# Performance work log

Measured on AMD Instinct MI355X. Metric: run time of the kernel, lower is better.

## Reference

```python
import jax, jax.numpy as jnp
import numpy as np
import math

B, S, D, H = 4, 2048, 1024, 16
DK = D // H  # 64
THETA = 10000.0


def setup_inputs() -> dict:
    key = jax.random.key(0)
    ks = jax.random.split(key, 5)
    std = 0.02
    return {
        "x": jax.random.normal(ks[0], (B, S, D), dtype=jnp.float32),
        "Wq": jax.random.normal(ks[1], (D, D), dtype=jnp.float32) * std,
        "Wk": jax.random.normal(ks[2], (D, D), dtype=jnp.float32) * std,
        "Wv": jax.random.normal(ks[3], (D, D), dtype=jnp.float32) * std,
        "Wo": jax.random.normal(ks[4], (D, D), dtype=jnp.float32) * std / math.sqrt(2 * 12),
        "token_positions": jnp.arange(S, dtype=jnp.int32),
    }


def _rope(x, pos):
    # x: [B, H, S, DK]; pos: [S]. Interleaved-pair rotary embedding.
    inv_freq = THETA ** (-jnp.arange(0, DK, 2, dtype=jnp.float32) / DK)  # [DK/2]
    ang = pos.astype(jnp.float32)[:, None] * inv_freq[None, :]  # [S, DK/2]
    cos, sin = jnp.cos(ang), jnp.sin(ang)
    x1, x2 = x[..., 0::2], x[..., 1::2]  # [B, H, S, DK/2]
    r1 = x1 * cos - x2 * sin
    r2 = x1 * sin + x2 * cos
    return jnp.stack([r1, r2], axis=-1).reshape(x.shape)


def reference(x, Wq, Wk, Wv, Wo, token_positions):
    b, s, d = x.shape
    Q = x @ Wq
    K = x @ Wk
    V = x @ Wv
    # [B, S, D] -> [B, H, S, DK]
    def split(t):
        return t.reshape(b, s, H, DK).transpose(0, 2, 1, 3)
    Qh, Kh, Vh = split(Q), split(K), split(V)
    Qh = _rope(Qh, token_positions)
    Kh = _rope(Kh, token_positions)
    scores = jnp.einsum('bhqd,bhkd->bhqk', Qh, Kh) / math.sqrt(DK)
    causal = jnp.tril(jnp.ones((s, s), dtype=bool))
    scores = jnp.where(causal, scores, -jnp.inf)
    probs = jax.nn.softmax(scores, axis=-1)
    out = jnp.einsum('bhqk,bhkd->bhqd', probs, Vh)
    out = out.transpose(0, 2, 1, 3).reshape(b, s, d)
    return out @ Wo
```

## Files before the change

kernel.cpp:

```cpp
#include <hip/hip_runtime.h>
#include <hip/hip_bf16.h>

#define B_N 4
#define S_LEN 2048
#define D_MODEL 1024
#define N_HEAD 16
#define D_HEAD 64
#define M_ROWS (B_N * S_LEN)

typedef short bf16x8 __attribute__((ext_vector_type(8)));
typedef short bf16x4 __attribute__((ext_vector_type(4)));
typedef float f32x4 __attribute__((ext_vector_type(4)));

#if __has_builtin(__builtin_amdgcn_mfma_f32_16x16x16bf16_1k)
#define HAVE_MFMA16 1
#else
#define HAVE_MFMA16 0
#endif

__device__ __forceinline__ unsigned short f2bf(float f) {
  union { float f; unsigned int u; } v; v.f = f;
  unsigned int r = v.u + 0x7FFFu + ((v.u >> 16) & 1u);
  return (unsigned short)(r >> 16);
}
__device__ __forceinline__ float bf2f(unsigned short u) {
  union { unsigned int u; float f; } v; v.u = ((unsigned int)u) << 16;
  return v.f;
}
__device__ __forceinline__ unsigned int pkbf(float a, float b) {
  union { __hip_bfloat162 h; unsigned int u; } cv;
  cv.h = __float22bfloat162_rn(make_float2(a, b));
  return cv.u;
}
__device__ __forceinline__ bf16x8 ld8(const unsigned short* p) {
  return *reinterpret_cast<const bf16x8*>(p);
}
__device__ __forceinline__ bf16x4 ld4(const unsigned short* p) {
  return *reinterpret_cast<const bf16x4*>(p);
}
__device__ __forceinline__ void glds16(const unsigned short* g, unsigned short* l) {
  __builtin_amdgcn_global_load_lds(
      (const __attribute__((address_space(1))) unsigned int*)g,
      (__attribute__((address_space(3))) unsigned int*)l, 16, 0, 0);
}

__global__ __launch_bounds__(256) void rope_tab_k(const int* __restrict__ pos,
                                                  float2* __restrict__ tab) {
  const int idx = blockIdx.x * 256 + threadIdx.x;
  const int s = idx >> 5;
  const int i = idx & 31;
  const float inv = exp2f(-(float)i * 0.41524101186092029f);
  const float ang = (float)pos[s] * inv;
  tab[idx] = make_float2(cosf(ang), sinf(ang));
}

__global__ __launch_bounds__(256) void cast_k(const float* __restrict__ X,
                                              unsigned short* __restrict__ Y) {
  const size_t i = ((size_t)blockIdx.x * 256 + threadIdx.x) * 8;
  const float4 a = *reinterpret_cast<const float4*>(X + i);
  const float4 b = *reinterpret_cast<const float4*>(X + i + 4);
  union { unsigned int u[4]; uint4 v; } o;
  o.u[0] = pkbf(a.x, a.y); o.u[1] = pkbf(a.z, a.w);
  o.u[2] = pkbf(b.x, b.y); o.u[3] = pkbf(b.z, b.w);
  *reinterpret_cast<uint4*>(Y + i) = o.v;
}

__global__ __launch_bounds__(256) void wtrans_k(
    const float* __restrict__ W0, const float* __restrict__ W1,
    const float* __restrict__ W2, const float* __restrict__ W3,
    unsigned short* __restrict__ T0, unsigned short* __restrict__ T1,
    unsigned short* __restrict__ T2, unsigned short* __restrict__ T3) {
  const int z = blockIdx.z;
  const float* __restrict__ W = (z == 0) ? W0 : (z == 1) ? W1 : (z == 2) ? W2 : W3;
  unsigned short* __restrict__ T = (z == 0) ? T0 : (z == 1) ? T1 : (z == 2) ? T2 : T3;
  __shared__ __align__(16) unsigned short tile[64][72];
  const int kb = blockIdx.x * 64;
  const int nb = blockIdx.y * 64;
#pragma unroll
  for (int it = 0; it < 2; ++it) {
    const int chunk = it * 256 + threadIdx.x;
    const int r = chunk >> 3;
    const int c8 = (chunk & 7) * 8;
    const float* src = W + (size_t)(kb + r) * D_MODEL + nb + c8;
    const float4 a = *reinterpret_cast<const float4*>(src);
    const float4 b = *reinterpret_cast<const float4*>(src + 4);
    union { unsigned int u[4]; uint4 v; } o;
    o.u[0] = pkbf(a.x, a.y); o.u[1] = pkbf(a.z, a.w);
    o.u[2] = pkbf(b.x, b.y); o.u[3] = pkbf(b.z, b.w);
    *reinterpret_cast<uint4*>(&tile[r][c8]) = o.v;
  }
  __syncthreads();
#pragma unroll
  for (int it = 0; it < 2; ++it) {
    const int chunk = it * 256 + threadIdx.x;
    const int n = chunk >> 3;
    const int k8 = (chunk & 7) * 8;
    __align__(16) unsigned short vals[8];
#pragma unroll
    for (int j = 0; j < 8; ++j) vals[j] = tile[k8 + j][n];
    *reinterpret_cast<uint4*>(T + (size_t)(nb + n) * D_MODEL + kb + k8) =
        *reinterpret_cast<const uint4*>(vals);
  }
}

__global__ __launch_bounds__(256) void gemm2_k(
    const unsigned short* __restrict__ A, const unsigned short* __restrict__ W,
    unsigned short* __restrict__ Qo, unsigned short* __restrict__ Ko,
    unsigned short* __restrict__ VTo, float* __restrict__ OF,
    const float2* __restrict__ tab, const int mode) {
  __shared__ __align__(16) unsigned short smem[4][64][68];
  unsigned short* As = &smem[0][0][0];
  unsigned short* Bs = As + 128 * 32;

  const int tid = threadIdx.x;
  const int lane = tid & 63;
  const int w = tid >> 6;
  const int l15 = lane & 15;
  const int l4 = lane >> 4;

  const int row0 = blockIdx.x * 128;
  const int col0 = blockIdx.y * 128;

  const int srow = w * 32 + (lane >> 2);
  const int scol = (lane & 3) * 8;
  const unsigned short* ga = A + (size_t)(row0 + srow) * D_MODEL + scol;
  const unsigned short* gb = W + (size_t)(col0 + srow) * D_MODEL + scol;
  unsigned short* la = &As[(w * 32) * 32];
  unsigned short* lb = &Bs[(w * 32) * 32];

  const int wrow = (w & 1) * 64;
  const int wcol = (w >> 1) * 64;

  f32x4 acc[4][4];
  const f32x4 fz = {0.f, 0.f, 0.f, 0.f};
#pragma unroll
  for (int m = 0; m < 4; ++m)
#pragma unroll
    for (int n = 0; n < 4; ++n) acc[m][n] = fz;

  for (int kb = 0; kb < D_MODEL; kb += 32) {
    glds16(ga + kb, la);
    glds16(ga + 16 * D_MODEL + kb, la + 16 * 32);
    glds16(gb + kb, lb);
    glds16(gb + 16 * D_MODEL + kb, lb + 16 * 32);
    __syncthreads();
    bf16x8 af[4], bfr[4];
#pragma unroll
    for (int m = 0; m < 4; ++m) af[m] = ld8(&As[(wrow + m * 16 + l15) * 32 + l4 * 8]);
#pragma unroll
    for (int n = 0; n < 4; ++n) bfr[n] = ld8(&Bs[(wcol + n * 16 + l15) * 32 + l4 * 8]);
#pragma unroll
    for (int m = 0; m < 4; ++m)
#pragma unroll
      for (int n = 0; n < 4; ++n)
        acc[m][n] = __builtin_amdgcn_mfma_f32_16x16x32_bf16(af[m], bfr[n], acc[m][n], 0, 0, 0);
    __syncthreads();
  }

  if (mode == 1) {
#pragma unroll
    for (int n = 0; n < 4; ++n) {
      const int gcol = col0 + wcol + n * 16 + l15;
#pragma unroll
      for (int m = 0; m < 4; ++m)
#pragma unroll
        for (int r = 0; r < 4; ++r)
          OF[(size_t)(row0 + wrow + m * 16 + l4 * 4 + r) * D_MODEL + gcol] = acc[m][n][r];
    }
    return;
  }

  unsigned short (*T)[68] = (unsigned short(*)[68]) & smem[w];
  const bool isV = (col0 >= 2048);
  if (!isV) {
#pragma unroll
    for (int m = 0; m < 4; ++m)
#pragma unroll
      for (int n = 0; n < 4; ++n)
#pragma unroll
        for (int r = 0; r < 4; ++r)
          T[m * 16 + l4 * 4 + r][n * 16 + l15] = f2bf(acc[m][n][r]);
  } else {
#pragma unroll
    for (int m = 0; m < 4; ++m)
#pragma unroll
      for (int n = 0; n < 4; ++n)
#pragma unroll
        for (int r = 0; r < 4; ++r)
          T[n * 16 + l15][m * 16 + l4 * 4 + r] = f2bf(acc[m][n][r]);
  }

  const int lr = lane >> 3;
  const int lc = lane & 7;
  if (!isV) {
    const bool isQ = (col0 < 1024);
    unsigned short* O = isQ ? Qo : Ko;
    const float qs = isQ ? 0.18033688011112042f : 1.0f;
    const int cbase = (col0 & 1023) + wcol;
#pragma unroll
    for (int rg = 0; rg < 8; ++rg) {
      const int trow = rg * 8 + lr;
      const int grow = row0 + wrow + trow;
      const int s = grow & (S_LEN - 1);
      const bf16x8 vv = ld8(&T[trow][lc * 8]);
      const float4 tA = *reinterpret_cast<const float4*>(&tab[s * 32 + lc * 4]);
      const float4 tB = *reinterpret_cast<const float4*>(&tab[s * 32 + lc * 4 + 2]);
      float x[8];
#pragma unroll
      for (int j = 0; j < 8; ++j) x[j] = bf2f((unsigned short)vv[j]);
      union { unsigned int u[4]; uint4 v; } o;
      o.u[0] = pkbf((x[0] * tA.x - x[1] * tA.y) * qs, (x[0] * tA.y + x[1] * tA.x) * qs);
      o.u[1] = pkbf((x[2] * tA.z - x[3] * tA.w) * qs, (x[2] * tA.w + x[3] * tA.z) * qs);
      o.u[2] = pkbf((x[4] * tB.x - x[5] * tB.y) * qs, (x[4] * tB.y + x[5] * tB.x) * qs);
      o.u[3] = pkbf((x[6] * tB.z - x[7] * tB.w) * qs, (x[6] * tB.w + x[7] * tB.z) * qs);
      *reinterpret_cast<uint4*>(O + (size_t)grow * D_MODEL + cbase + lc * 8) = o.v;
    }
  } else {
    const int vc0 = (col0 - 2048) + wcol;
    const int h = vc0 >> 6;
    const int b = row0 >> 11;
    const int s0 = (row0 & (S_LEN - 1)) + wrow;
#pragma unroll
    for (int rg = 0; rg < 8; ++rg) {
      const int dk = rg * 8 + lr;
      const bf16x8 vv = ld8(&T[dk][lc * 8]);
      *reinterpret_cast<bf16x8*>(
          VTo + ((size_t)((b << 4) + h) * 64 + dk) * S_LEN + s0 + lc * 8) = vv;
    }
  }
}

__global__ __launch_bounds__(512) void attn6_k(
    const unsigned short* __restrict__ Q, const unsigned short* __restrict__ K,
    const unsigned short* __restrict__ VT, unsigned short* __restrict__ O) {
  const int pair = blockIdx.x;
  const int h = blockIdx.y;
  const int b = blockIdx.z;
  const int tid = threadIdx.x;
  const int w = tid >> 6;
  const int lane = tid & 63;
  const int l15 = lane & 15;
  const int l4 = lane >> 4;

  __shared__ __align__(16) unsigned short Ks[64][72];
  __shared__ __align__(16) unsigned short Vs[64][72];
#if !HAVE_MFMA16
  __shared__ __align__(16) unsigned short Ps[8][16][72];
#endif

  const f32x4 fz = {0.f, 0.f, 0.f, 0.f};
  const unsigned short* kbase = K + (size_t)b * S_LEN * D_MODEL + h * D_HEAD;
  const unsigned short* vbase = VT + (size_t)((b << 4) + h) * 64 * S_LEN;

  const int rr = tid >> 3;
  const int c8 = (tid & 7) * 8;

  for (int half = 0; half < 2; ++half) {
    const int qt = half ? (15 - pair) : pair;
    const int qb = qt * 128;
    const int qw0 = qb + w * 16;

    bf16x8 qf[2];
#pragma unroll
    for (int kc = 0; kc < 2; ++kc)
      qf[kc] = ld8(Q + (size_t)(b * S_LEN + qw0 + l15) * D_MODEL +
                   h * D_HEAD + kc * 32 + l4 * 8);

    f32x4 o[4];
#pragma unroll
    for (int d = 0; d < 4; ++d) o[d] = fz;
    float lsum = 0.f;

    const int nkt = qb / 64 + 2;
    uint4 kreg = *reinterpret_cast<const uint4*>(kbase + (size_t)rr * D_MODEL + c8);
    uint4 vreg = *reinterpret_cast<const uint4*>(vbase + (size_t)rr * S_LEN + c8);

    for (int kt = 0; kt < nkt; ++kt) {
      const int kb0 = kt * 64;
      *reinterpret_cast<uint4*>(&Ks[rr][c8]) = kreg;
      *reinterpret_cast<uint4*>(&Vs[rr][c8]) = vreg;
      if (kt + 1 < nkt) {
        const int nb0 = kb0 + 64;
        kreg = *reinterpret_cast<const uint4*>(kbase + (size_t)(nb0 + rr) * D_MODEL + c8);
        vreg = *reinterpret_cast<const uint4*>(vbase + (size_t)rr * S_LEN + nb0 + c8);
      }
      __syncthreads();

      if (kb0 <= qw0 + 15) {
        f32x4 s[4];
#pragma unroll
        for (int n = 0; n < 4; ++n) {
          const bf16x8 kf0 = ld8(&Ks[n * 16 + l15][l4 * 8]);
          const bf16x8 kf1 = ld8(&Ks[n * 16 + l15][32 + l4 * 8]);
          f32x4 a0 = __builtin_amdgcn_mfma_f32_16x16x32_bf16(kf0, qf[0], fz, 0, 0, 0);
          s[n] = __builtin_amdgcn_mfma_f32_16x16x32_bf16(kf1, qf[1], a0, 0, 0, 0);
        }
        bf16x4 pf[4];
        const bool full = (kb0 + 63 <= qw0);
        const int q = qw0 + l15;
        float su = lsum;
#pragma unroll
        for (int n = 0; n < 4; ++n) {
          float e[4];
          if (full) {
#pragma unroll
            for (int r = 0; r < 4; ++r) e[r] = exp2f(s[n][r]);
          } else {
#pragma unroll
            for (int r = 0; r < 4; ++r) {
              const int key = kb0 + n * 16 + l4 * 4 + r;
              const float v = exp2f(s[n][r]);
              e[r] = (key <= q) ? v : 0.f;
            }
          }
          su += (e[0] + e[1]) + (e[2] + e[3]);
          union { unsigned int u[2]; bf16x4 v; } pk;
          pk.u[0] = pkbf(e[0], e[1]);
          pk.u[1] = pkbf(e[2], e[3]);
          pf[n] = pk.v;
        }
        lsum = su;

#if HAVE_MFMA16
#pragma unroll
        for (int d = 0; d < 4; ++d) {
          bf16x4 vfc[4];
#pragma unroll
          for (int c = 0; c < 4; ++c) vfc[c] = ld4(&Vs[d * 16 + l15][c * 16 + l4 * 4]);
#pragma unroll
          for (int c = 0; c < 4; ++c)
            o[d] = __builtin_amdgcn_mfma_f32_16x16x16bf16_1k(vfc[c], pf[c], o[d], 0, 0, 0);
        }
#else
#pragma unroll
        for (int n = 0; n < 4; ++n)
          *reinterpret_cast<bf16x4*>(&Ps[w][l15][n * 16 + l4 * 4]) = pf[n];
        bf16x8 pfr[2];
#pragma unroll
        for (int kc = 0; kc < 2; ++kc)
          pfr[kc] = ld8(&Ps[w][l15][kc * 32 + l4 * 8]);
#pragma unroll
        for (int d = 0; d < 4; ++d) {
          const bf16x8 vf0 = ld8(&Vs[d * 16 + l15][l4 * 8]);
          const bf16x8 vf1 = ld8(&Vs[d * 16 + l15][32 + l4 * 8]);
          o[d] = __builtin_amdgcn_mfma_f32_16x16x32_bf16(vf0, pfr[0], o[d], 0, 0, 0);
          o[d] = __builtin_amdgcn_mfma_f32_16x16x32_bf16(vf1, pfr[1], o[d], 0, 0, 0);
        }
#endif
      }
      __syncthreads();
    }

    float s = lsum;
    s += __shfl_xor(s, 16);
    s += __shfl_xor(s, 32);
    const float li = 1.0f / s;
    unsigned short* op = O + (size_t)(b * S_LEN + qw0 + l15) * D_MODEL +
                         h * D_HEAD + l4 * 4;
#pragma unroll
    for (int d = 0; d < 4; ++d) {
      union { unsigned int u[2]; uint2 v; } ov;
      ov.u[0] = pkbf(o[d][0] * li, o[d][1] * li);
      ov.u[1] = pkbf(o[d][2] * li, o[d][3] * li);
      *reinterpret_cast<uint2*>(op + d * 16) = ov.v;
    }
  }
}

extern "C" void kernel_launch(void* const* d_in, const int* in_sizes, int n_in,
                              void* d_out, int out_size, void* d_ws, size_t ws_size,
                              hipStream_t stream) {
  const float* x  = (const float*)d_in[0];
  const float* Wq = (const float*)d_in[1];
  const float* Wk = (const float*)d_in[2];
  const float* Wv = (const float*)d_in[3];
  const float* Wo = (const float*)d_in[4];
  const int* pos  = (const int*)d_in[5];
  float* out = (float*)d_out;

  char* ws = (char*)d_ws;
  const size_t big = (size_t)M_ROWS * D_MODEL * 2;
  const size_t wsz = (size_t)D_MODEL * D_MODEL * 2;
  unsigned short* xb  = (unsigned short*)(ws + 0 * big);
  unsigned short* Qb  = (unsigned short*)(ws + 1 * big);
  unsigned short* Kb  = (unsigned short*)(ws + 2 * big);
  unsigned short* VT  = (unsigned short*)(ws + 3 * big);
  unsigned short* Wqkvt = (unsigned short*)(ws + 4 * big);
  unsigned short* Wot   = (unsigned short*)(ws + 4 * big + 3 * wsz);
  float2* tab = (float2*)d_out;

  rope_tab_k<<<dim3(S_LEN * 32 / 256), 256, 0, stream>>>(pos, tab);
  cast_k<<<dim3(M_ROWS * D_MODEL / 2048), 256, 0, stream>>>(x, xb);
  wtrans_k<<<dim3(16, 16, 4), 256, 0, stream>>>(
      Wq, Wk, Wv, Wo, Wqkvt, Wqkvt + (size_t)D_MODEL * D_MODEL,
      Wqkvt + 2 * (size_t)D_MODEL * D_MODEL, Wot);
  gemm2_k<<<dim3(M_ROWS / 128, 3 * D_MODEL / 128), 256, 0, stream>>>(
      xb, Wqkvt, Qb, Kb, VT, nullptr, tab, 0);
  attn6_k<<<dim3(8, N_HEAD, B_N), 512, 0, stream>>>(Qb, Kb, VT, Qb);
  gemm2_k<<<dim3(M_ROWS / 128, D_MODEL / 128), 256, 0, stream>>>(
      Qb, Wot, nullptr, nullptr, nullptr, out, nullptr, 1);
}
```

Before: 278.8 us.

## Add 256x256-tile pipelined QKV GEMM kernel with direct-to-LDS loads

```diff
diff --git a/kernel.cpp b/kernel.cpp
--- a/kernel.cpp
+++ b/kernel.cpp
@@ -169,65 +169,176 @@
     }
     return;
   }
-
-  unsigned short (*T)[68] = (unsigned short(*)[68]) & smem[w];
-  const bool isV = (col0 >= 2048);
-  if (!isV) {
-#pragma unroll
-    for (int m = 0; m < 4; ++m)
-#pragma unroll
-      for (int n = 0; n < 4; ++n)
-#pragma unroll
-        for (int r = 0; r < 4; ++r)
-          T[m * 16 + l4 * 4 + r][n * 16 + l15] = f2bf(acc[m][n][r]);
-  } else {
-#pragma unroll
-    for (int m = 0; m < 4; ++m)
-#pragma unroll
-      for (int n = 0; n < 4; ++n)
-#pragma unroll
-        for (int r = 0; r < 4; ++r)
-          T[n * 16 + l15][m * 16 + l4 * 4 + r] = f2bf(acc[m][n][r]);
-  }
-
+}
+
+__global__ __launch_bounds__(512, 2) void gemm8_k(
+    const unsigned short* __restrict__ A, const unsigned short* __restrict__ W,
+    unsigned short* __restrict__ Qo, unsigned short* __restrict__ Ko,
+    unsigned short* __restrict__ VTo, const float2* __restrict__ tab) {
+  __shared__ __align__(16) unsigned short smem[2][2][256 * 64];
+
+  const int tid = threadIdx.x;
+  const int lane = tid & 63;
+  const int w = tid >> 6;
+  const int l15 = lane & 15;
+  const int l4 = lane >> 4;
+  const int wm = w >> 2;
+  const int wn = w & 3;
+
+  const int row0 = blockIdx.x * 256;
+  const int col0 = blockIdx.y * 256;
+
+  const int srow = lane >> 3;
+  const int schunk = (lane & 7) ^ ((lane >> 4) & 2);
+  const unsigned short* gA = A + (size_t)(row0 + w * 8 + srow) * D_MODEL + schunk * 8;
+  const unsigned short* gB = W + (size_t)(col0 + w * 8 + srow) * D_MODEL + schunk * 8;
+
+  const int kx = (l15 & 4) ? 16 : 0;
+  const int kc0 = (l4 * 8) ^ kx;
+  const int kc1 = (32 + l4 * 8) ^ kx;
+
+  f32x4 acc[8][4];
+  const f32x4 fz = {0.f, 0.f, 0.f, 0.f};
+#pragma unroll
+  for (int m = 0; m < 8; ++m)
+#pragma unroll
+    for (int n = 0; n < 4; ++n) acc[m][n] = fz;
+
+#define G8_STAGE(SL, T)                                                        \
+  do {                                                                         \
+    asm volatile("" ::: "memory");                                             \
+    const size_t ko_ = (size_t)(T) * 64;                                       \
+    unsigned short* sa_ = &smem[SL][0][w * 512];                               \
+    unsigned short* sb_ = &smem[SL][1][w * 512];                               \
+    _Pragma("unroll") for (int j = 0; j < 4; ++j) {                            \
+      glds16(gA + ko_ + (size_t)j * 64 * D_MODEL, sa_ + j * 4096);             \
+      glds16(gB + ko_ + (size_t)j * 64 * D_MODEL, sb_ + j * 4096);             \
+    }                                                                          \
+    asm volatile("" ::: "memory");                                             \
+  } while (0)
+
+#define G8_PHASE(SL, MH, NH)                                                   \
+  do {                                                                         \
+    const unsigned short* As_ = &smem[SL][0][0];                               \
+    const unsigned short* Bs_ = &smem[SL][1][0];                               \
+    bf16x8 af_[4][2], bf_[2][2];                                               \
+    _Pragma("unroll") for (int mi = 0; mi < 4; ++mi) {                         \
+      const int rr_ = (wm * 128 + ((MH) * 4 + mi) * 16 + l15) * 64;            \
+      af_[mi][0] = ld8(As_ + rr_ + kc0);                                       \
+      af_[mi][1] = ld8(As_ + rr_ + kc1);                                       \
+    }                                                                          \
+    _Pragma("unroll") for (int ni = 0; ni < 2; ++ni) {                         \
+      const int cc_ = (wn * 64 + ((NH) * 2 + ni) * 16 + l15) * 64;             \
+      bf_[ni][0] = ld8(Bs_ + cc_ + kc0);                                       \
+      bf_[ni][1] = ld8(Bs_ + cc_ + kc1);                                       \
+    }                                                                          \
+    __builtin_amdgcn_s_barrier();                                              \
+    __builtin_amdgcn_s_setprio(1);                                             \
+    _Pragma("unroll") for (int mi = 0; mi < 4; ++mi)                           \
+      _Pragma("unroll") for (int ni = 0; ni < 2; ++ni) {                       \
+        acc[(MH) * 4 + mi][(NH) * 2 + ni] =                                    \
+            __builtin_amdgcn_mfma_f32_16x16x32_bf16(                           \
+                af_[mi][0], bf_[ni][0], acc[(MH) * 4 + mi][(NH) * 2 + ni],     \
+                0, 0, 0);                                                      \
+        acc[(MH) * 4 + mi][(NH) * 2 + ni] =                                    \
+            __builtin_amdgcn_mfma_f32_16x16x32_bf16(                           \
+                af_[mi][1], bf_[ni][1], acc[(MH) * 4 + mi][(NH) * 2 + ni],     \
+                0, 0, 0);                                                      \
+      }                                                                        \
+    __builtin_amdgcn_s_setprio(0);                                             \
+    __builtin_amdgcn_s_barrier();                                              \
+  } while (0)
+
+  G8_STAGE(0, 0);
+  G8_STAGE(1, 1);
+
+  for (int i = 0; i < 8; ++i) {
+    asm volatile("s_waitcnt vmcnt(8)" ::: "memory");
+    __builtin_amdgcn_s_barrier();
+    G8_PHASE(0, 0, 0);
+    G8_PHASE(0, 0, 1);
+    G8_PHASE(0, 1, 0);
+    G8_PHASE(0, 1, 1);
+    if (i < 7) {
+      G8_STAGE(0, 2 * i + 2);
+      asm volatile("s_waitcnt vmcnt(8)" ::: "memory");
+    } else {
+      asm volatile("s_waitcnt vmcnt(0)" ::: "memory");
+    }
+    __builtin_amdgcn_s_barrier();
+    G8_PHASE(1, 0, 0);
+    G8_PHASE(1, 0, 1);
+    G8_PHASE(1, 1, 0);
+    G8_PHASE(1, 1, 1);
+    if (i < 7) G8_STAGE(1, 2 * i + 3);
+  }
+  asm volatile("" ::: "memory");
+
+  unsigned short(*T)[68] =
+      (unsigned short(*)[68])(&smem[0][0][0] + w * 4352);
+  const int gcb = col0 + wn * 64;
+  const bool isV = (gcb >= 2048);
   const int lr = lane >> 3;
   const int lc = lane & 7;
-  if (!isV) {
-    const bool isQ = (col0 < 1024);
-    unsigned short* O = isQ ? Qo : Ko;
-    const float qs = isQ ? 0.18033688011112042f : 1.0f;
-    const int cbase = (col0 & 1023) + wcol;
-#pragma unroll
-    for (int rg = 0; rg < 8; ++rg) {
-      const int trow = rg * 8 + lr;
-      const int grow = row0 + wrow + trow;
-      const int s = grow & (S_LEN - 1);
-      const bf16x8 vv = ld8(&T[trow][lc * 8]);
-      const float4 tA = *reinterpret_cast<const float4*>(&tab[s * 32 + lc * 4]);
-      const float4 tB = *reinterpret_cast<const float4*>(&tab[s * 32 + lc * 4 + 2]);
-      float x[8];
-#pragma unroll
-      for (int j = 0; j < 8; ++j) x[j] = bf2f((unsigned short)vv[j]);
-      union { unsigned int u[4]; uint4 v; } o;
-      o.u[0] = pkbf((x[0] * tA.x - x[1] * tA.y) * qs, (x[0] * tA.y + x[1] * tA.x) * qs);
-      o.u[1] = pkbf((x[2] * tA.z - x[3] * tA.w) * qs, (x[2] * tA.w + x[3] * tA.z) * qs);
-      o.u[2] = pkbf((x[4] * tB.x - x[5] * tB.y) * qs, (x[4] * tB.y + x[5] * tB.x) * qs);
-      o.u[3] = pkbf((x[6] * tB.z - x[7] * tB.w) * qs, (x[6] * tB.w + x[7] * tB.z) * qs);
-      *reinterpret_cast<uint4*>(O + (size_t)grow * D_MODEL + cbase + lc * 8) = o.v;
+
+#pragma unroll
+  for (int p = 0; p < 2; ++p) {
+    if (!isV) {
+#pragma unroll
+      for (int mi = 0; mi < 4; ++mi)
+#pragma unroll
+        for (int n = 0; n < 4; ++n)
+#pragma unroll
+          for (int r = 0; r < 4; ++r)
+            T[mi * 16 + l4 * 4 + r][n * 16 + l15] = f2bf(acc[p * 4 + mi][n][r]);
+    } else {
+#pragma unroll
+      for (int mi = 0; mi < 4; ++mi)
+#pragma unroll
+        for (int n = 0; n < 4; ++n)
+#pragma unroll
+          for (int r = 0; r < 4; ++r)
+            T[n * 16 + l15][mi * 16 + l4 * 4 + r] = f2bf(acc[p * 4 + mi][n][r]);
     }
-  } else {
-    const int vc0 = (col0 - 2048) + wcol;
-    const int h = vc0 >> 6;
-    const int b = row0 >> 11;
-    const int s0 = (row0 & (S_LEN - 1)) + wrow;
-#pragma unroll
-    for (int rg = 0; rg < 8; ++rg) {
-      const int dk = rg * 8 + lr;
-      const bf16x8 vv = ld8(&T[dk][lc * 8]);
-      *reinterpret_cast<bf16x8*>(
-          VTo + ((size_t)((b << 4) + h) * 64 + dk) * S_LEN + s0 + lc * 8) = vv;
+    if (!isV) {
+      const bool isQ = (gcb < 1024);
+      unsigned short* O = isQ ? Qo : Ko;
+      const float qs = isQ ? 0.18033688011112042f : 1.0f;
+      const int cbase = gcb & 1023;
+#pragma unroll
+      for (int rg = 0; rg < 8; ++rg) {
+        const int trow = rg * 8 + lr;
+        const int grow = row0 + wm * 128 + p * 64 + trow;
+        const int s = grow & (S_LEN - 1);
+        const bf16x8 vv = ld8(&T[trow][lc * 8]);
+        const float4 tA = *reinterpret_cast<const float4*>(&tab[s * 32 + lc * 4]);
+        const float4 tB = *reinterpret_cast<const float4*>(&tab[s * 32 + lc * 4 + 2]);
+        float x[8];
+#pragma unroll
+        for (int j = 0; j < 8; ++j) x[j] = bf2f((unsigned short)vv[j]);
+        union { unsigned int u[4]; uint4 v; } o;
+        o.u[0] = pkbf((x[0] * tA.x - x[1] * tA.y) * qs, (x[0] * tA.y + x[1] * tA.x) * qs);
+        o.u[1] = pkbf((x[2] * tA.z - x[3] * tA.w) * qs, (x[2] * tA.w + x[3] * tA.z) * qs);
+        o.u[2] = pkbf((x[4] * tB.x - x[5] * tB.y) * qs, (x[4] * tB.y + x[5] * tB.x) * qs);
+        o.u[3] = pkbf((x[6] * tB.z - x[7] * tB.w) * qs, (x[6] * tB.w + x[7] * tB.z) * qs);
+        *reinterpret_cast<uint4*>(O + (size_t)grow * D_MODEL + cbase + lc * 8) = o.v;
+      }
+    } else {
+      const int vc0 = gcb - 2048;
+      const int h = vc0 >> 6;
+      const int bb = row0 >> 11;
+      const int s0 = (row0 & (S_LEN - 1)) + wm * 128 + p * 64;
+#pragma unroll
+      for (int rg = 0; rg < 8; ++rg) {
+        const int dk = rg * 8 + lr;
+        const bf16x8 vv = ld8(&T[dk][lc * 8]);
+        *reinterpret_cast<bf16x8*>(
+            VTo + ((size_t)((bb << 4) + h) * 64 + dk) * S_LEN + s0 + lc * 8) = vv;
+      }
     }
   }
+#undef G8_STAGE
+#undef G8_PHASE
 }
 
 __global__ __launch_bounds__(512) void attn6_k(
@@ -394,8 +505,8 @@
   wtrans_k<<<dim3(16, 16, 4), 256, 0, stream>>>(
       Wq, Wk, Wv, Wo, Wqkvt, Wqkvt + (size_t)D_MODEL * D_MODEL,
       Wqkvt + 2 * (size_t)D_MODEL * D_MODEL, Wot);
-  gemm2_k<<<dim3(M_ROWS / 128, 3 * D_MODEL / 128), 256, 0, stream>>>(
-      xb, Wqkvt, Qb, Kb, VT, nullptr, tab, 0);
+  gemm8_k<<<dim3(M_ROWS / 256, 3 * D_MODEL / 256), 512, 0, stream>>>(
+      xb, Wqkvt, Qb, Kb, VT, tab);
   attn6_k<<<dim3(8, N_HEAD, B_N), 512, 0, stream>>>(Qb, Kb, VT, Qb);
   gemm2_k<<<dim3(M_ROWS / 128, D_MODEL / 128), 256, 0, stream>>>(
       Qb, Wot, nullptr, nullptr, nullptr, out, nullptr, 1);
```

New measurement: 295.6 us. +6.0%, slower.

## Add triple-buffered 128x256 QKV GEMM kernel with swizzled LDS and split phases

Applied to the files above, without the earlier changes.

```diff
diff --git a/kernel.cpp b/kernel.cpp
--- a/kernel.cpp
+++ b/kernel.cpp
@@ -105,9 +105,7 @@
 
 __global__ __launch_bounds__(256) void gemm2_k(
     const unsigned short* __restrict__ A, const unsigned short* __restrict__ W,
-    unsigned short* __restrict__ Qo, unsigned short* __restrict__ Ko,
-    unsigned short* __restrict__ VTo, float* __restrict__ OF,
-    const float2* __restrict__ tab, const int mode) {
+    float* __restrict__ OF) {
   __shared__ __align__(16) unsigned short smem[4][64][68];
   unsigned short* As = &smem[0][0][0];
   unsigned short* Bs = As + 128 * 32;
@@ -157,50 +155,146 @@
     __syncthreads();
   }
 
-  if (mode == 1) {
-#pragma unroll
-    for (int n = 0; n < 4; ++n) {
-      const int gcol = col0 + wcol + n * 16 + l15;
-#pragma unroll
-      for (int m = 0; m < 4; ++m)
-#pragma unroll
-        for (int r = 0; r < 4; ++r)
-          OF[(size_t)(row0 + wrow + m * 16 + l4 * 4 + r) * D_MODEL + gcol] = acc[m][n][r];
-    }
-    return;
-  }
-
-  unsigned short (*T)[68] = (unsigned short(*)[68]) & smem[w];
-  const bool isV = (col0 >= 2048);
-  if (!isV) {
+#pragma unroll
+  for (int n = 0; n < 4; ++n) {
+    const int gcol = col0 + wcol + n * 16 + l15;
 #pragma unroll
     for (int m = 0; m < 4; ++m)
 #pragma unroll
-      for (int n = 0; n < 4; ++n)
-#pragma unroll
-        for (int r = 0; r < 4; ++r)
-          T[m * 16 + l4 * 4 + r][n * 16 + l15] = f2bf(acc[m][n][r]);
-  } else {
-#pragma unroll
-    for (int m = 0; m < 4; ++m)
-#pragma unroll
-      for (int n = 0; n < 4; ++n)
-#pragma unroll
-        for (int r = 0; r < 4; ++r)
-          T[n * 16 + l15][m * 16 + l4 * 4 + r] = f2bf(acc[m][n][r]);
-  }
-
+      for (int r = 0; r < 4; ++r)
+        OF[(size_t)(row0 + wrow + m * 16 + l4 * 4 + r) * D_MODEL + gcol] = acc[m][n][r];
+  }
+}
+
+__global__ __launch_bounds__(512, 1) void gemm8_k(
+    const unsigned short* __restrict__ A, const unsigned short* __restrict__ W,
+    unsigned short* __restrict__ Qo, unsigned short* __restrict__ Ko,
+    unsigned short* __restrict__ VTo, const float2* __restrict__ tab) {
+  __shared__ __align__(16) unsigned short smem[3][384 * 64];
+
+  const int tid = threadIdx.x;
+  const int lane = tid & 63;
+  const int w = tid >> 6;
+  const int l15 = lane & 15;
+  const int l4 = lane >> 4;
+  const int wm = w >> 2;
+  const int wn = w & 3;
+
+  const int row0 = blockIdx.x * 128;
+  const int col0 = blockIdx.y * 256;
+
+  const int srow = lane >> 3;
+  const int schunk = (lane & 7) ^ srow;
+  const unsigned short* gA = A + (size_t)(row0 + w * 8 + srow) * D_MODEL + schunk * 8;
+  const unsigned short* gB = W + (size_t)(col0 + w * 8 + srow) * D_MODEL + schunk * 8;
+
+  const int swz = l15 & 7;
+  const int kc0 = ((l4) ^ swz) * 8;
+  const int kc1 = ((l4 + 4) ^ swz) * 8;
+
+  f32x4 acc[4][4];
+  const f32x4 fz = {0.f, 0.f, 0.f, 0.f};
+#pragma unroll
+  for (int m = 0; m < 4; ++m)
+#pragma unroll
+    for (int n = 0; n < 4; ++n) acc[m][n] = fz;
+
+#define G8_STAGE_A(SL, T)                                                      \
+  do {                                                                         \
+    unsigned short* sa_ = &smem[SL][(w * 8) * 64];                             \
+    const unsigned short* g_ = gA + (size_t)(T) * 64;                          \
+    glds16(g_, sa_);                                                           \
+    glds16(g_ + 64 * D_MODEL, sa_ + 64 * 64);                                  \
+  } while (0)
+
+#define G8_STAGE_B(SL, T)                                                      \
+  do {                                                                         \
+    unsigned short* sb_ = &smem[SL][(128 + w * 8) * 64];                       \
+    const unsigned short* g_ = gB + (size_t)(T) * 64;                          \
+    glds16(g_, sb_);                                                           \
+    glds16(g_ + 64 * D_MODEL, sb_ + 64 * 64);                                  \
+    glds16(g_ + 128 * D_MODEL, sb_ + 128 * 64);                                \
+    glds16(g_ + 192 * D_MODEL, sb_ + 192 * 64);                                \
+  } while (0)
+
+#define G8_PHASE(SL, KC, STG)                                                  \
+  do {                                                                         \
+    const unsigned short* As_ = &smem[SL][0];                                  \
+    const unsigned short* Bs_ = &smem[SL][128 * 64];                           \
+    bf16x8 af_[4], bf_[4];                                                     \
+    _Pragma("unroll") for (int mi = 0; mi < 4; ++mi)                           \
+      af_[mi] = ld8(As_ + (wm * 64 + mi * 16 + l15) * 64 + (KC));              \
+    _Pragma("unroll") for (int ni = 0; ni < 4; ++ni)                           \
+      bf_[ni] = ld8(Bs_ + (wn * 64 + ni * 16 + l15) * 64 + (KC));              \
+    STG;                                                                       \
+    __builtin_amdgcn_s_barrier();                                              \
+    __builtin_amdgcn_s_setprio(1);                                             \
+    _Pragma("unroll") for (int mi = 0; mi < 4; ++mi)                           \
+      _Pragma("unroll") for (int ni = 0; ni < 4; ++ni)                         \
+        acc[mi][ni] = __builtin_amdgcn_mfma_f32_16x16x32_bf16(                 \
+            af_[mi], bf_[ni], acc[mi][ni], 0, 0, 0);                           \
+    __builtin_amdgcn_s_setprio(0);                                             \
+    __builtin_amdgcn_s_barrier();                                              \
+  } while (0)
+
+  G8_STAGE_A(0, 0); G8_STAGE_B(0, 0);
+  G8_STAGE_A(1, 1); G8_STAGE_B(1, 1);
+
+#pragma unroll
+  for (int t = 0; t < 16; ++t) {
+    const int sl = t % 3;
+    const int sp = (t + 2) % 3;
+    if (t < 15) {
+      asm volatile("s_waitcnt vmcnt(6)" ::: "memory");
+    } else {
+      asm volatile("s_waitcnt vmcnt(0)" ::: "memory");
+    }
+    __builtin_amdgcn_s_barrier();
+    if (t < 14) {
+      G8_PHASE(sl, kc0, G8_STAGE_A(sp, (t + 2)));
+      G8_PHASE(sl, kc1, G8_STAGE_B(sp, (t + 2)));
+    } else {
+      G8_PHASE(sl, kc0, ((void)0));
+      G8_PHASE(sl, kc1, ((void)0));
+    }
+  }
+#undef G8_STAGE_A
+#undef G8_STAGE_B
+#undef G8_PHASE
+
+  unsigned short(*T)[68] =
+      (unsigned short(*)[68])(&smem[0][0] + w * 4352);
+  const int gcb = col0 + wn * 64;
+  const bool isV = (gcb >= 2048);
   const int lr = lane >> 3;
   const int lc = lane & 7;
+
   if (!isV) {
-    const bool isQ = (col0 < 1024);
+#pragma unroll
+    for (int mi = 0; mi < 4; ++mi)
+#pragma unroll
+      for (int n = 0; n < 4; ++n)
+#pragma unroll
+        for (int r = 0; r < 4; ++r)
+          T[mi * 16 + l4 * 4 + r][n * 16 + l15] = f2bf(acc[mi][n][r]);
+  } else {
+#pragma unroll
+    for (int mi = 0; mi < 4; ++mi)
+#pragma unroll
+      for (int n = 0; n < 4; ++n)
+#pragma unroll
+        for (int r = 0; r < 4; ++r)
+          T[n * 16 + l15][mi * 16 + l4 * 4 + r] = f2bf(acc[mi][n][r]);
+  }
+  if (!isV) {
+    const bool isQ = (gcb < 1024);
     unsigned short* O = isQ ? Qo : Ko;
     const float qs = isQ ? 0.18033688011112042f : 1.0f;
-    const int cbase = (col0 & 1023) + wcol;
+    const int cbase = gcb & 1023;
 #pragma unroll
     for (int rg = 0; rg < 8; ++rg) {
       const int trow = rg * 8 + lr;
-      const int grow = row0 + wrow + trow;
+      const int grow = row0 + wm * 64 + trow;
       const int s = grow & (S_LEN - 1);
       const bf16x8 vv = ld8(&T[trow][lc * 8]);
       const float4 tA = *reinterpret_cast<const float4*>(&tab[s * 32 + lc * 4]);
@@ -216,16 +310,16 @@
       *reinterpret_cast<uint4*>(O + (size_t)grow * D_MODEL + cbase + lc * 8) = o.v;
     }
   } else {
-    const int vc0 = (col0 - 2048) + wcol;
+    const int vc0 = gcb - 2048;
     const int h = vc0 >> 6;
-    const int b = row0 >> 11;
-    const int s0 = (row0 & (S_LEN - 1)) + wrow;
+    const int bb = row0 >> 11;
+    const int s0 = (row0 & (S_LEN - 1)) + wm * 64;
 #pragma unroll
     for (int rg = 0; rg < 8; ++rg) {
       const int dk = rg * 8 + lr;
       const bf16x8 vv = ld8(&T[dk][lc * 8]);
       *reinterpret_cast<bf16x8*>(
-          VTo + ((size_t)((b << 4) + h) * 64 + dk) * S_LEN + s0 + lc * 8) = vv;
+          VTo + ((size_t)((bb << 4) + h) * 64 + dk) * S_LEN + s0 + lc * 8) = vv;
     }
   }
 }
@@ -394,9 +488,8 @@
   wtrans_k<<<dim3(16, 16, 4), 256, 0, stream>>>(
       Wq, Wk, Wv, Wo, Wqkvt, Wqkvt + (size_t)D_MODEL * D_MODEL,
       Wqkvt + 2 * (size_t)D_MODEL * D_MODEL, Wot);
-  gemm2_k<<<dim3(M_ROWS / 128, 3 * D_MODEL / 128), 256, 0, stream>>>(
-      xb, Wqkvt, Qb, Kb, VT, nullptr, tab, 0);
+  gemm8_k<<<dim3(M_ROWS / 128, 3 * D_MODEL / 256), 512, 0, stream>>>(
+      xb, Wqkvt, Qb, Kb, VT, tab);
   attn6_k<<<dim3(8, N_HEAD, B_N), 512, 0, stream>>>(Qb, Kb, VT, Qb);
-  gemm2_k<<<dim3(M_ROWS / 128, D_MODEL / 128), 256, 0, stream>>>(
-      Qb, Wot, nullptr, nullptr, nullptr, out, nullptr, 1);
-}
+  gemm2_k<<<dim3(M_ROWS / 128, D_MODEL / 128), 256, 0, stream>>>(Qb, Wot, out);
+}
```

Result: faster. 270.0 us (median of 2 runs) (-3.2%).
